# Kernel tuning notes

Hardware: AMD Instinct MI355X
Metric: run time of the kernel (lower is better)

The kernel has to match this reference:

```python
import jax, jax.numpy as jnp
import numpy as np

B = 32768          # rays
N = 512            # gaussians
NSH = 4            # -> m = 2*NSH+1 = 9 SH coeffs
H = 512.0
W = 512.0
S_MIN = 1.0 / 30.0       # 1 / n_gaussian_max_pixels
S_MAX = 1.0 / 0.75       # 1 / n_gaussian_min_pixels
MU_BORDER = 1.05
PI_APPROX = 3.1416       # matches the literal in the torch source


def setup_inputs() -> dict:
    key = jax.random.key(0)
    ks = jax.random.split(key, 6)
    # pixel coordinates in [0, W) x [0, H)
    x = jax.random.uniform(ks[0], (B, 2), jnp.float32) * jnp.array([W, H], jnp.float32)
    rgbsh = jax.random.uniform(ks[1], (N, 2 * NSH + 1, 3), jnp.float32)
    opacity = jax.random.uniform(ks[2], (N,), jnp.float32)
    mu = jax.random.uniform(ks[3], (N, 2), jnp.float32) * 2.0 - 1.0
    scale = jax.random.uniform(ks[4], (N, 2), jnp.float32)
    angle = jax.random.uniform(ks[5], (N,), jnp.float32) * 2.0 - 1.0
    return {"x": x, "rgbsh": rgbsh, "opacity": opacity,
            "mu": mu, "scale": scale, "angle": angle}


def _forward(x, rgbsh, opacity, mu, scale, angle):
    wh = jnp.array([W, H], x.dtype)                      # (2,)
    xnorm = x / wh * 2.0 - 1.0                           # (B,2) in [-1,1]
    gmu = jnp.tanh(mu) * MU_BORDER                       # (N,2)
    S = jnp.clip(scale, 0.0, 1.0) * (S_MAX - S_MIN) + S_MIN  # (N,2) inverse radii

    # pixel-space offset ray->gaussian: (x - mu)/2 * (w,h)
    vec = (xnorm[:, None, :] - gmu[None, :, :]) * (wh * 0.5)   # (B,N,2)

    # validity mask (computed under no_grad in torch): |S * vec| < 5
    dist = jnp.linalg.norm(vec * S[None], axis=-1)             # (B,N)
    valid = jax.lax.stop_gradient(dist < 5.0)

    # per-gaussian rotation matrices
    alpha = jnp.tanh(angle) * PI_APPROX                        # (N,)
    c, s = jnp.cos(alpha), jnp.sin(alpha)
    R = jnp.stack([jnp.stack([c, -s], -1),
                   jnp.stack([s,  c], -1)], axis=-2)           # (N,2,2)

    # Mahalanobis-like squared distance: || R @ diag(S) @ vec ||^2
    svec = vec * S[None]                                       # (B,N,2)
    rot = jnp.einsum('nij,bnj->bni', R, svec)                  # (B,N,2)
    d2 = jnp.sum(rot * rot, axis=-1)                           # (B,N)

    # view angle in the gaussian frame
    vnorm = vec / (1e-10 + jnp.linalg.norm(vec, axis=-1, keepdims=True))
    vrot = jnp.einsum('nij,bnj->bni', R, vnorm)                # (B,N,2)
    theta = jnp.arctan2(vrot[..., 0], vrot[..., 1])            # (B,N)

    # 2D SH basis: [1, sin(t), cos(t), sin(2t), cos(2t), ...]
    basis = [jnp.ones_like(theta)]
    for i in range(NSH):
        basis.append(jnp.sin(theta * (i + 1)))
        basis.append(jnp.cos(theta * (i + 1)))
    basis = jnp.stack(basis, axis=-1)                          # (B,N,M)

    rgb = jax.nn.sigmoid(jnp.einsum('bnm,nmc->bnc', basis, rgbsh))  # (B,N,3)
    wgt = jnp.where(valid,
                    jnp.exp(-d2) * jax.nn.sigmoid(opacity)[None, :],
                    jnp.zeros((), x.dtype))                    # (B,N)

    # accumulate_along_rays: per-ray weighted sum over gaussians
    return jnp.einsum('bn,bnc->bc', wgt, rgb)                  # (B,3)


def reference(x, rgbsh, opacity, mu, scale, angle):
    return _forward(x, rgbsh, opacity, mu, scale, angle)
```

## Files before the change

kernel.cpp:

```cpp
#include <hip/hip_runtime.h>

#define BDIM 1024
#define NW   16
#define RPB  64
#define NG   512
#define GPW  (NG / NW)


__global__ void pre_kernel(const float* __restrict__ rgbsh,
                           const float* __restrict__ opacity,
                           const float* __restrict__ mu,
                           const float* __restrict__ scale,
                           const float* __restrict__ angle,
                           float4* __restrict__ wsA,
                           float4* __restrict__ wsB,
                           float4* __restrict__ wsSh,
                           int N)
{
    int n = blockIdx.x * blockDim.x + threadIdx.x;
    if (n >= N) return;
    const float S_MIN = 1.0f / 30.0f;
    const float S_MAX = 1.0f / 0.75f;
    float gmx = tanhf(mu[2 * n + 0]) * 1.05f;
    float gmy = tanhf(mu[2 * n + 1]) * 1.05f;
    float Sx = fminf(fmaxf(scale[2 * n + 0], 0.0f), 1.0f) * (S_MAX - S_MIN) + S_MIN;
    float Sy = fminf(fmaxf(scale[2 * n + 1], 0.0f), 1.0f) * (S_MAX - S_MIN) + S_MIN;
    float ax = 256.0f * Sx, ay = 256.0f * Sy;
    wsA[n] = make_float4(ax, ay, -gmx * ax, -gmy * ay);
    float a = tanhf(angle[n]) * 3.1416f;
    float sa, ca;
    sincosf(a, &sa, &ca);
    float w0 = 1.0f / (1.0f + expf(-opacity[n]));
    wsB[n] = make_float4(ca, sa, w0, 1.0f / Sx);
    const float* sh = rgbsh + n * 27;
    float buf[28];
    #pragma unroll
    for (int q = 0; q < 27; ++q) buf[q] = sh[q];
    buf[27] = 1.0f / Sy;
    #pragma unroll
    for (int q = 0; q < 7; ++q)
        wsSh[n * 7 + q] = make_float4(buf[4*q], buf[4*q+1], buf[4*q+2], buf[4*q+3]);
}

__global__ __launch_bounds__(BDIM, 8) void splat_kernel(
    const float*  __restrict__ x,
    const float4* __restrict__ wsA,
    const float4* __restrict__ wsB,
    const float4* __restrict__ wsSh,
    float* __restrict__ out,
    int B)
{
    __shared__ float4 gA[NG];
    __shared__ float4 gB[NG];
    __shared__ float  acc[NW][RPB * 3];
    const int tid = threadIdx.x;

    if (tid < NG)          gA[tid]      = wsA[tid];
    else                   gB[tid - NG] = wsB[tid - NG];
    __syncthreads();

    const int lane = tid & 63;
    const int w    = tid >> 6;
    const int b    = blockIdx.x * RPB + lane;
    const int bb   = (b < B) ? b : (B - 1);
    float2 p2 = *(const float2*)(x + 2 * bb);
    float pnx = p2.x * (1.0f / 256.0f) - 1.0f;
    float pny = p2.y * (1.0f / 256.0f) - 1.0f;

    float accR = 0.0f, accG = 0.0f, accB = 0.0f;
    const int g0 = w * GPW;

    #pragma unroll 4
    for (int j = 0; j < GPW; ++j) {
        const int g = g0 + j;
        float4 pa = gA[g];
        float sx = fmaf(pnx, pa.x, pa.z);
        float sy = fmaf(pny, pa.y, pa.w);
        float t  = fmaf(sx, sx, sy * sy);
        bool  v  = t < 25.0f;
        if (__any(v)) {
            if (v) {
                float4 q = gB[g];
                const int gu = __builtin_amdgcn_readfirstlane(g);
                const float4* sh = wsSh + gu * 7;
                float4 h6 = sh[6];
                float c = q.x, s = q.y;
                float rx = fmaf(c, sx, -s * sy);
                float ry = fmaf(s, sx,  c * sy);
                float d2 = fmaf(rx, rx, ry * ry);
                float vx  = sx * q.w;
                float vy  = sy * h6.w;
                float len = sqrtf(fmaf(vx, vx, vy * vy));
                float inv = __builtin_amdgcn_rcpf(1e-10f + len);
                float rvx = fmaf(c, vx, -s * vy);
                float rvy = fmaf(s, vx,  c * vy);
                float s1 = rvx * inv, c1 = rvy * inv;
                float s2 = 2.0f * s1 * c1;
                float c2 = fmaf(c1, c1, -s1 * s1);
                float s3 = fmaf(s2, c1,  c2 * s1);
                float c3 = fmaf(c2, c1, -s2 * s1);
                float s4 = 2.0f * s2 * c2;
                float c4 = fmaf(c2, c2, -s2 * s2);
                float4 h0 = sh[0], h1 = sh[1], h2 = sh[2];
                float4 h3 = sh[3], h4 = sh[4], h5 = sh[5];
                float rr = h0.x, gg = h0.y, bb2 = h0.z;
                rr = fmaf(s1, h0.w, rr);  gg = fmaf(s1, h1.x, gg);  bb2 = fmaf(s1, h1.y, bb2);
                rr = fmaf(c1, h1.z, rr);  gg = fmaf(c1, h1.w, gg);  bb2 = fmaf(c1, h2.x, bb2);
                rr = fmaf(s2, h2.y, rr);  gg = fmaf(s2, h2.z, gg);  bb2 = fmaf(s2, h2.w, bb2);
                rr = fmaf(c2, h3.x, rr);  gg = fmaf(c2, h3.y, gg);  bb2 = fmaf(c2, h3.z, bb2);
                rr = fmaf(s3, h3.w, rr);  gg = fmaf(s3, h4.x, gg);  bb2 = fmaf(s3, h4.y, bb2);
                rr = fmaf(c3, h4.z, rr);  gg = fmaf(c3, h4.w, gg);  bb2 = fmaf(c3, h5.x, bb2);
                rr = fmaf(s4, h5.y, rr);  gg = fmaf(s4, h5.z, gg);  bb2 = fmaf(s4, h5.w, bb2);
                rr = fmaf(c4, h6.x, rr);  gg = fmaf(c4, h6.y, gg);  bb2 = fmaf(c4, h6.z, bb2);
                rr  = __builtin_amdgcn_rcpf(1.0f + __expf(-rr));
                gg  = __builtin_amdgcn_rcpf(1.0f + __expf(-gg));
                bb2 = __builtin_amdgcn_rcpf(1.0f + __expf(-bb2));
                float wt = __expf(-d2) * q.z;
                accR = fmaf(wt, rr,  accR);
                accG = fmaf(wt, gg,  accG);
                accB = fmaf(wt, bb2, accB);
            }
        }
    }

    acc[w][lane * 3 + 0] = accR;
    acc[w][lane * 3 + 1] = accG;
    acc[w][lane * 3 + 2] = accB;
    __syncthreads();
    if (tid < RPB * 3) {
        float s = 0.0f;
        #pragma unroll
        for (int w2 = 0; w2 < NW; ++w2)
            s += acc[w2][tid];
        const int idx = blockIdx.x * (RPB * 3) + tid;
        if (idx < 3 * B)
            out[idx] = s;
    }
}

extern "C" void kernel_launch(void* const* d_in, const int* in_sizes, int n_in,
                              void* d_out, int out_size, void* d_ws, size_t ws_size,
                              hipStream_t stream) {
    const float* x       = (const float*)d_in[0];
    const float* rgbsh   = (const float*)d_in[1];
    const float* opacity = (const float*)d_in[2];
    const float* mu      = (const float*)d_in[3];
    const float* scale   = (const float*)d_in[4];
    const float* angle   = (const float*)d_in[5];
    float* out = (float*)d_out;

    const int B = in_sizes[0] / 2;
    const int N = in_sizes[2];

    char* ws = (char*)d_ws;
    float4* wsA  = (float4*)(ws);
    float4* wsB  = (float4*)(ws + (size_t)N * 16);
    float4* wsSh = (float4*)(ws + (size_t)N * 32);

    pre_kernel<<<(N + 255) / 256, 256, 0, stream>>>(rgbsh, opacity, mu, scale,
                                                    angle, wsA, wsB, wsSh, N);
    splat_kernel<<<(B + RPB - 1) / RPB, BDIM, 0, stream>>>(x, wsA, wsB, wsSh,
                                                           out, B);
}
```

Measured before the change: 77.16 us.

## Drop LDS staging and read wave-uniform gaussian params via scalar loads

Removes the shared-memory staging of per-gaussian params and the block-wide barrier. The splat loop now reads them straight from global memory with wave-uniform addresses, which the compiler can turn into scalar (SMEM) loads. The rotation, opacity, inverse scales and SH coefficients are packed into one 32-float record per gaussian, so each visible gaussian is fetched from a single contiguous line. The loop unroll drops from 4 to 2. The tradeoff is relying on the scalar cache instead of LDS, with possible extra latency on each gaussian test.

```diff
diff --git a/kernel.cpp b/kernel.cpp
--- a/kernel.cpp
+++ b/kernel.cpp
@@ -13,8 +13,7 @@
                            const float* __restrict__ scale,
                            const float* __restrict__ angle,
                            float4* __restrict__ wsA,
-                           float4* __restrict__ wsB,
-                           float4* __restrict__ wsSh,
+                           float*  __restrict__ wsH,
                            int N)
 {
     int n = blockIdx.x * blockDim.x + threadIdx.x;
@@ -30,66 +29,56 @@
     float a = tanhf(angle[n]) * 3.1416f;
     float sa, ca;
     sincosf(a, &sa, &ca);
-    float w0 = 1.0f / (1.0f + expf(-opacity[n]));
-    wsB[n] = make_float4(ca, sa, w0, 1.0f / Sx);
-    const float* sh = rgbsh + n * 27;
-    float buf[28];
+    float* hp = wsH + ((size_t)n << 5);
+    hp[0] = ca;
+    hp[1] = sa;
+    hp[2] = 1.0f / (1.0f + expf(-opacity[n]));
+    hp[3] = 1.0f / Sx;
+    hp[4] = 1.0f / Sy;
     #pragma unroll
-    for (int q = 0; q < 27; ++q) buf[q] = sh[q];
-    buf[27] = 1.0f / Sy;
-    #pragma unroll
-    for (int q = 0; q < 7; ++q)
-        wsSh[n * 7 + q] = make_float4(buf[4*q], buf[4*q+1], buf[4*q+2], buf[4*q+3]);
+    for (int q = 0; q < 27; ++q) hp[5 + q] = rgbsh[n * 27 + q];
 }
 
 __global__ __launch_bounds__(BDIM, 8) void splat_kernel(
     const float*  __restrict__ x,
     const float4* __restrict__ wsA,
-    const float4* __restrict__ wsB,
-    const float4* __restrict__ wsSh,
+    const float*  __restrict__ wsH,
     float* __restrict__ out,
     int B)
 {
-    __shared__ float4 gA[NG];
-    __shared__ float4 gB[NG];
-    __shared__ float  acc[NW][RPB * 3];
-    const int tid = threadIdx.x;
+    __shared__ float acc[NW][RPB * 3];
+    const int tid  = threadIdx.x;
+    const int lane = tid & 63;
+    const int w = __builtin_amdgcn_readfirstlane(tid >> 6);
 
-    if (tid < NG)          gA[tid]      = wsA[tid];
-    else                   gB[tid - NG] = wsB[tid - NG];
-    __syncthreads();
-
-    const int lane = tid & 63;
-    const int w    = tid >> 6;
-    const int b    = blockIdx.x * RPB + lane;
-    const int bb   = (b < B) ? b : (B - 1);
+    const int b  = blockIdx.x * RPB + lane;
+    const int bb = (b < B) ? b : (B - 1);
     float2 p2 = *(const float2*)(x + 2 * bb);
     float pnx = p2.x * (1.0f / 256.0f) - 1.0f;
     float pny = p2.y * (1.0f / 256.0f) - 1.0f;
 
     float accR = 0.0f, accG = 0.0f, accB = 0.0f;
-    const int g0 = w * GPW;
+    const float4* __restrict__ wA = wsA + w * GPW;
+    const float*  __restrict__ wH = wsH + ((size_t)(w * GPW) << 5);
 
-    #pragma unroll 4
+    #pragma unroll 2
     for (int j = 0; j < GPW; ++j) {
-        const int g = g0 + j;
-        float4 pa = gA[g];
+        float4 pa = wA[j];
         float sx = fmaf(pnx, pa.x, pa.z);
         float sy = fmaf(pny, pa.y, pa.w);
         float t  = fmaf(sx, sx, sy * sy);
         bool  v  = t < 25.0f;
         if (__any(v)) {
+            const float* hp = wH + (j << 5);
+            float c   = hp[0], s = hp[1];
+            float w0  = hp[2];
+            float iSx = hp[3], iSy = hp[4];
             if (v) {
-                float4 q = gB[g];
-                const int gu = __builtin_amdgcn_readfirstlane(g);
-                const float4* sh = wsSh + gu * 7;
-                float4 h6 = sh[6];
-                float c = q.x, s = q.y;
                 float rx = fmaf(c, sx, -s * sy);
                 float ry = fmaf(s, sx,  c * sy);
                 float d2 = fmaf(rx, rx, ry * ry);
-                float vx  = sx * q.w;
-                float vy  = sy * h6.w;
+                float vx  = sx * iSx;
+                float vy  = sy * iSy;
                 float len = sqrtf(fmaf(vx, vx, vy * vy));
                 float inv = __builtin_amdgcn_rcpf(1e-10f + len);
                 float rvx = fmaf(c, vx, -s * vy);
@@ -101,21 +90,20 @@
                 float c3 = fmaf(c2, c1, -s2 * s1);
                 float s4 = 2.0f * s2 * c2;
                 float c4 = fmaf(c2, c2, -s2 * s2);
-                float4 h0 = sh[0], h1 = sh[1], h2 = sh[2];
-                float4 h3 = sh[3], h4 = sh[4], h5 = sh[5];
-                float rr = h0.x, gg = h0.y, bb2 = h0.z;
-                rr = fmaf(s1, h0.w, rr);  gg = fmaf(s1, h1.x, gg);  bb2 = fmaf(s1, h1.y, bb2);
-                rr = fmaf(c1, h1.z, rr);  gg = fmaf(c1, h1.w, gg);  bb2 = fmaf(c1, h2.x, bb2);
-                rr = fmaf(s2, h2.y, rr);  gg = fmaf(s2, h2.z, gg);  bb2 = fmaf(s2, h2.w, bb2);
-                rr = fmaf(c2, h3.x, rr);  gg = fmaf(c2, h3.y, gg);  bb2 = fmaf(c2, h3.z, bb2);
-                rr = fmaf(s3, h3.w, rr);  gg = fmaf(s3, h4.x, gg);  bb2 = fmaf(s3, h4.y, bb2);
-                rr = fmaf(c3, h4.z, rr);  gg = fmaf(c3, h4.w, gg);  bb2 = fmaf(c3, h5.x, bb2);
-                rr = fmaf(s4, h5.y, rr);  gg = fmaf(s4, h5.z, gg);  bb2 = fmaf(s4, h5.w, bb2);
-                rr = fmaf(c4, h6.x, rr);  gg = fmaf(c4, h6.y, gg);  bb2 = fmaf(c4, h6.z, bb2);
+                const float* sh = hp + 5;
+                float rr = sh[0], gg = sh[1], bb2 = sh[2];
+                rr = fmaf(s1, sh[ 3], rr);  gg = fmaf(s1, sh[ 4], gg);  bb2 = fmaf(s1, sh[ 5], bb2);
+                rr = fmaf(c1, sh[ 6], rr);  gg = fmaf(c1, sh[ 7], gg);  bb2 = fmaf(c1, sh[ 8], bb2);
+                rr = fmaf(s2, sh[ 9], rr);  gg = fmaf(s2, sh[10], gg);  bb2 = fmaf(s2, sh[11], bb2);
+                rr = fmaf(c2, sh[12], rr);  gg = fmaf(c2, sh[13], gg);  bb2 = fmaf(c2, sh[14], bb2);
+                rr = fmaf(s3, sh[15], rr);  gg = fmaf(s3, sh[16], gg);  bb2 = fmaf(s3, sh[17], bb2);
+                rr = fmaf(c3, sh[18], rr);  gg = fmaf(c3, sh[19], gg);  bb2 = fmaf(c3, sh[20], bb2);
+                rr = fmaf(s4, sh[21], rr);  gg = fmaf(s4, sh[22], gg);  bb2 = fmaf(s4, sh[23], bb2);
+                rr = fmaf(c4, sh[24], rr);  gg = fmaf(c4, sh[25], gg);  bb2 = fmaf(c4, sh[26], bb2);
                 rr  = __builtin_amdgcn_rcpf(1.0f + __expf(-rr));
                 gg  = __builtin_amdgcn_rcpf(1.0f + __expf(-gg));
                 bb2 = __builtin_amdgcn_rcpf(1.0f + __expf(-bb2));
-                float wt = __expf(-d2) * q.z;
+                float wt = __expf(-d2) * w0;
                 accR = fmaf(wt, rr,  accR);
                 accG = fmaf(wt, gg,  accG);
                 accB = fmaf(wt, bb2, accB);
@@ -153,12 +141,10 @@
     const int N = in_sizes[2];
 
     char* ws = (char*)d_ws;
-    float4* wsA  = (float4*)(ws);
-    float4* wsB  = (float4*)(ws + (size_t)N * 16);
-    float4* wsSh = (float4*)(ws + (size_t)N * 32);
+    float4* wsA = (float4*)(ws);
+    float*  wsH = (float*)(ws + (size_t)N * 16);
 
     pre_kernel<<<(N + 255) / 256, 256, 0, stream>>>(rgbsh, opacity, mu, scale,
-                                                    angle, wsA, wsB, wsSh, N);
-    splat_kernel<<<(B + RPB - 1) / RPB, BDIM, 0, stream>>>(x, wsA, wsB, wsSh,
-                                                           out, B);
+                                                    angle, wsA, wsH, N);
+    splat_kernel<<<(B + RPB - 1) / RPB, BDIM, 0, stream>>>(x, wsA, wsH, out, B);
 }
```

After: 77.29 us. Within noise of the previous version (+0.2%).
